# Optimization experiments

Hardware: AMD Instinct MI355X
Metric: run time of the kernel (lower is better)

## Reference

```python
import jax, jax.numpy as jnp
from jax import lax
import numpy as np

B, T, V, H = 64, 256, 4096, 512


def setup_inputs() -> dict:
    key = jax.random.key(0)
    k1, k2, k3, k4 = jax.random.split(key, 4)
    x = jax.random.randint(k1, (B, T), 0, V, dtype=jnp.int32)
    # RNNScratch params (std=0.01 normal init, as in the LM head)
    Wxh = 0.01 * jax.random.normal(k2, (V, H), dtype=jnp.float32)
    Whh = 0.01 * jax.random.normal(k3, (H, H), dtype=jnp.float32)
    bh = jnp.zeros((H,), dtype=jnp.float32)
    Wo = 0.01 * jax.random.normal(k4, (H, V), dtype=jnp.float32)
    Bo = jnp.zeros((V,), dtype=jnp.float32)
    return {"x": x, "Wxh": Wxh, "Whh": Whh, "bh": bh, "Wo": Wo, "Bo": Bo}


def reference(x, Wxh, Whh, bh, Wo, Bo):
    # one_hot(x).float() @ Wxh is exactly a row gather from Wxh
    xs = jnp.take(Wxh, x.T, axis=0)  # [T, B, H]
    h0 = jnp.zeros((x.shape[0], Whh.shape[0]), dtype=Wxh.dtype)

    def step(h, xt):
        h = jnp.tanh(xt + h @ Whh + bh)  # [B, H]
        return h, h

    _, hs = lax.scan(step, h0, xs)  # hs: [T, B, H]
    # per-step output projection, fused into one einsum over time
    out = jnp.einsum("tbh,hv->btv", hs, Wo) + Bo  # [B, T, V]
    return out
```

## Files before the change

kernel.cpp:

```cpp
#include <hip/hip_runtime.h>


typedef __fp16 half2_t __attribute__((ext_vector_type(2)));
typedef __attribute__((ext_vector_type(8))) short short8;
typedef __attribute__((ext_vector_type(4))) float f32x4;

__device__ __forceinline__ unsigned short f32_to_bf16(float f) {
  unsigned int u = __builtin_bit_cast(unsigned int, f);
  u = (u + 0x7FFFu + ((u >> 16) & 1u)) >> 16;
  return (unsigned short)u;
}

__device__ __forceinline__ unsigned int pack_f16x2(float a, float b) {
  half2_t h = __builtin_amdgcn_cvt_pkrtz(a, b);
  return __builtin_bit_cast(unsigned int, h);
}

__device__ __forceinline__ float fdot2_(unsigned int w, unsigned int h, float acc) {
  return __builtin_amdgcn_fdot2(__builtin_bit_cast(half2_t, w),
                                __builtin_bit_cast(half2_t, h), acc, false);
}

__device__ __forceinline__ void glds16(const void* g, void* lds) {
  __builtin_amdgcn_global_load_lds(
      (const __attribute__((address_space(1))) unsigned int*)g,
      (__attribute__((address_space(3))) unsigned int*)lds, 16, 0, 0);
}

__global__ __launch_bounds__(256) void pack_whhB(const float* __restrict__ Whh,
                                                 unsigned int* __restrict__ WhhB,
                                                 unsigned long long* __restrict__ hG64) {
  int idx = blockIdx.x * 256 + threadIdx.x;
  int e = idx & 3;
  int G = idx >> 2;
  int c = G & 127;
  int u = (G >> 7) & 15;
  int q = (G >> 11) & 3;
  int s = G >> 13;
  int p = q * 64 + u * 4 + e;
  int j = s * 128 + c;
  float f0 = Whh[(2 * p) * 512 + j];
  float f1 = Whh[(2 * p + 1) * 512 + j];
  WhhB[idx] = pack_f16x2(f0, f1);
  if (idx < 32768) hG64[idx] = 0ull;
}

__global__ __launch_bounds__(256) void transpose_wo(const float* __restrict__ Wo,
                                                    unsigned short* __restrict__ WoT) {
  __shared__ float tile[64][65];
  const int tv = blockIdx.x;
  const int th = blockIdx.y;
  const int tid = threadIdx.x;
  const int c = tid & 63, r4 = tid >> 6;
#pragma unroll
  for (int p = 0; p < 16; ++p) {
    int hl = p * 4 + r4;
    tile[hl][c] = Wo[(size_t)(th * 64 + hl) * 4096 + tv * 64 + c];
  }
  __syncthreads();
#pragma unroll
  for (int p = 0; p < 16; ++p) {
    int vl = p * 4 + r4;
    WoT[(size_t)(tv * 64 + vl) * 512 + th * 64 + c] = f32_to_bf16(tile[c][vl]);
  }
}

#define DOTK(kc_, A) do { \
  const uint4 w_ = wlds[(kc_) * 128 + c]; \
  const uint4 h_ = hbuf[(kc_)]; \
  A = fdot2_(w_.x, h_.x, A); A = fdot2_(w_.y, h_.y, A); \
  A = fdot2_(w_.z, h_.z, A); A = fdot2_(w_.w, h_.w, A); } while (0)

__global__ __launch_bounds__(512) void rnn_scanD(const int* __restrict__ x,
                                                 const float* __restrict__ Wxh,
                                                 const unsigned int* __restrict__ WhhB,
                                                 const float* __restrict__ bh,
                                                 unsigned short* __restrict__ hs,
                                                 unsigned long long* hG64) {
  __shared__ uint4 wlds[8192];
  __shared__ uint4 hbuf[64];
  __shared__ float pbuf[512];
  __shared__ int toks[256];
  const int bid = blockIdx.x;
  const int s = bid & 3;
  const int b = bid >> 2;
  const int tid = threadIdx.x;
  const int c = tid & 127;
  const int q = tid >> 7;
  const int s16 = s * 16;
  const uint4* W4 = (const uint4*)WhhB;

#pragma unroll
  for (int it = 0; it < 16; ++it) {
    int L = it * 512 + tid;
    wlds[L] = W4[s * 8192 + L];
  }
  if (tid < 64) hbuf[tid] = make_uint4(0u, 0u, 0u, 0u);
  if (tid < 256) toks[tid] = x[b * 256 + tid];
  __syncthreads();

  unsigned int* hb32 = (unsigned int*)hbuf;
  const float bhj = (tid < 128) ? bh[s * 128 + tid] : 0.f;

  for (int t = 0; t < 256; ++t) {
    const int tok = toks[t];
    const float xv = (tid < 128) ? Wxh[(size_t)tok * 512 + s * 128 + tid] : 0.f;

    float a0 = 0.f, a1 = 0.f, a2 = 0.f, a3 = 0.f;
    DOTK(s16 + 0 + q, a0); DOTK(s16 + 4 + q, a1);
    DOTK(s16 + 8 + q, a2); DOTK(s16 + 12 + q, a3);

    if (t > 0 && tid < 192) {
      const int r = (tid < s * 64) ? tid : tid + 64;
      const unsigned long long* src =
          hG64 + (((size_t)(t & 1)) << 14) + b * 256 + r;
      unsigned long long v;
      do {
        v = __hip_atomic_load(src, __ATOMIC_RELAXED, __HIP_MEMORY_SCOPE_AGENT);
      } while ((unsigned)(v >> 32) != (unsigned)t);
      half2_t up = __builtin_bit_cast(half2_t, (unsigned)v);
      hb32[r] = pack_f16x2(tanhf((float)up.x), tanhf((float)up.y));
    }
    __syncthreads();

    {
      int m1 = ((s + 1) & 3) * 16;
      DOTK(m1 + 0 + q, a0); DOTK(m1 + 4 + q, a1);
      DOTK(m1 + 8 + q, a2); DOTK(m1 + 12 + q, a3);
      int m2 = ((s + 2) & 3) * 16;
      DOTK(m2 + 0 + q, a0); DOTK(m2 + 4 + q, a1);
      DOTK(m2 + 8 + q, a2); DOTK(m2 + 12 + q, a3);
      int m3 = ((s + 3) & 3) * 16;
      DOTK(m3 + 0 + q, a0); DOTK(m3 + 4 + q, a1);
      DOTK(m3 + 8 + q, a2); DOTK(m3 + 12 + q, a3);
    }
    pbuf[q * 128 + c] = (a0 + a1) + (a2 + a3);
    __syncthreads();

    if (tid < 128) {
      const float ssum = pbuf[tid] + pbuf[tid + 128] + pbuf[tid + 256] + pbuf[tid + 384];
      const float u1 = xv + ssum + bhj;
      const float u2 = __shfl_down(u1, 1);
      if (!(tid & 1)) {
        const unsigned int up = pack_f16x2(u1, u2);
        __hip_atomic_store(
            hG64 + (((size_t)((t + 1) & 1)) << 14) + b * 256 + 64 * s + (tid >> 1),
            ((unsigned long long)(unsigned)(t + 1) << 32) | up,
            __ATOMIC_RELAXED, __HIP_MEMORY_SCOPE_AGENT);
        half2_t uo = __builtin_bit_cast(half2_t, up);
        const float h1 = tanhf((float)uo.x);
        const float h2 = tanhf((float)uo.y);
        hb32[64 * s + (tid >> 1)] = pack_f16x2(h1, h2);
        ((unsigned int*)hs)[(size_t)(b * 256 + t) * 256 + 64 * s + (tid >> 1)] =
            (unsigned int)f32_to_bf16(h1) | ((unsigned int)f32_to_bf16(h2) << 16);
      }
    }
    __syncthreads();
  }
}

__global__ __launch_bounds__(256) void gemm_out(const unsigned short* __restrict__ A,
                                                const unsigned short* __restrict__ Bt,
                                                const float* __restrict__ Bo,
                                                float* __restrict__ C) {
  __shared__ alignas(16) unsigned short As[128 * 32];
  __shared__ alignas(16) unsigned short Bs[128 * 32];
  const int tid = threadIdx.x;
  const int lane = tid & 63, wid = tid >> 6;
  const int bn = blockIdx.x & 31, bm = blockIdx.x >> 5;
  const int wr = wid >> 1, wc = wid & 1;

  f32x4 acc[4][4] = {};

  const unsigned short* Ag = A + (size_t)(bm * 128 + (tid >> 2)) * 512 + (tid & 3) * 8;
  const unsigned short* Bg = Bt + (size_t)(bn * 128 + (tid >> 2)) * 512 + (tid & 3) * 8;
  char* AsW = (char*)As + wid * 1024;
  char* BsW = (char*)Bs + wid * 1024;

  const int laneRow = lane & 15;
  const int k0 = (lane >> 4) * 8;

  for (int kt = 0; kt < 16; ++kt) {
    __syncthreads();
    const unsigned short* a0 = Ag + kt * 32;
    const unsigned short* b0 = Bg + kt * 32;
    glds16(a0,            AsW);
    glds16(a0 + 64 * 512, AsW + 4096);
    glds16(b0,            BsW);
    glds16(b0 + 64 * 512, BsW + 4096);
    __syncthreads();

    short8 af[4], bf[4];
#pragma unroll
    for (int f = 0; f < 4; ++f)
      af[f] = *(const short8*)&As[(wr * 64 + f * 16 + laneRow) * 32 + k0];
#pragma unroll
    for (int f = 0; f < 4; ++f)
      bf[f] = *(const short8*)&Bs[(wc * 64 + f * 16 + laneRow) * 32 + k0];
#pragma unroll
    for (int fm = 0; fm < 4; ++fm)
#pragma unroll
      for (int fn = 0; fn < 4; ++fn)
        acc[fm][fn] = __builtin_amdgcn_mfma_f32_16x16x32_bf16(af[fm], bf[fn], acc[fm][fn], 0, 0, 0);
  }

  const int mg0 = bm * 128 + wr * 64, ng0 = bn * 128 + wc * 64;
#pragma unroll
  for (int fn = 0; fn < 4; ++fn) {
    const int col = ng0 + fn * 16 + laneRow;
    const float bo = Bo[col];
#pragma unroll
    for (int fm = 0; fm < 4; ++fm) {
      const int row0 = mg0 + fm * 16 + (lane >> 4) * 4;
#pragma unroll
      for (int r = 0; r < 4; ++r)
        C[(size_t)(row0 + r) * 4096 + col] = acc[fm][fn][r] + bo;
    }
  }
}

extern "C" void kernel_launch(void* const* d_in, const int* in_sizes, int n_in,
                              void* d_out, int out_size, void* d_ws, size_t ws_size,
                              hipStream_t stream) {
  (void)in_sizes; (void)n_in; (void)out_size; (void)ws_size;
  const int* x = (const int*)d_in[0];
  const float* Wxh = (const float*)d_in[1];
  const float* Whh = (const float*)d_in[2];
  const float* bh = (const float*)d_in[3];
  const float* Wo = (const float*)d_in[4];
  const float* Bo = (const float*)d_in[5];
  float* out = (float*)d_out;

  unsigned int* WhhB = (unsigned int*)d_ws;
  unsigned short* WoT = (unsigned short*)((char*)d_ws + 524288);
  unsigned short* hs = (unsigned short*)((char*)d_ws + 4718592);
  unsigned long long* hG64 = (unsigned long long*)((char*)d_ws + 21495808);

  hipLaunchKernelGGL(pack_whhB, dim3(512), dim3(256), 0, stream, Whh, WhhB, hG64);
  hipLaunchKernelGGL(transpose_wo, dim3(64, 8), dim3(256), 0, stream, Wo, WoT);
  hipLaunchKernelGGL(rnn_scanD, dim3(256), dim3(512), 0, stream, x, Wxh, WhhB, bh,
                     hs, hG64);
  hipLaunchKernelGGL(gemm_out, dim3(4096), dim3(256), 0, stream, hs, WoT, Bo, out);
}
```

Before: 518.0 us.

## Quantize Whh to fp8 e5m2 and split recurrence across two blocks per batch

Packs Whh as 8-bit e5m2 values, which halves its size, so each block can hold 256 output columns of Whh in LDS. The recurrent scan then uses 2 blocks per batch row instead of 4, and less cross-block handoff is needed each time step. At dot time the fp8 bytes are widened to fp16 by shifting and masking before fdot2. The work is split so one half of the threads computes the local-h contribution while the other half polls the peer block's partial sums. This trades accuracy of Whh, since e5m2 keeps only two mantissa bits, for less inter-block synchronization and fewer launched blocks.

```diff
diff --git a/kernel.cpp b/kernel.cpp
--- a/kernel.cpp
+++ b/kernel.cpp
@@ -27,21 +27,29 @@
       (__attribute__((address_space(3))) unsigned int*)lds, 16, 0, 0);
 }
 
-__global__ __launch_bounds__(256) void pack_whhB(const float* __restrict__ Whh,
-                                                 unsigned int* __restrict__ WhhB,
+__device__ __forceinline__ unsigned int q8_e5m2(float f) {
+  _Float16 hv = (_Float16)f;
+  unsigned short u = __builtin_bit_cast(unsigned short, hv);
+  return (unsigned int)(((unsigned int)u + 0x7Fu + ((u >> 8) & 1u)) >> 8) & 0xFFu;
+}
+
+__global__ __launch_bounds__(256) void pack_whhE(const float* __restrict__ Whh,
+                                                 unsigned int* __restrict__ WhhE,
                                                  unsigned long long* __restrict__ hG64) {
   int idx = blockIdx.x * 256 + threadIdx.x;
-  int e = idx & 3;
+  int d = idx & 3;
   int G = idx >> 2;
-  int c = G & 127;
-  int u = (G >> 7) & 15;
-  int q = (G >> 11) & 3;
+  int c = G & 255;
+  int u = (G >> 8) & 15;
+  int q2 = (G >> 12) & 1;
   int s = G >> 13;
-  int p = q * 64 + u * 4 + e;
-  int j = s * 128 + c;
-  float f0 = Whh[(2 * p) * 512 + j];
-  float f1 = Whh[(2 * p + 1) * 512 + j];
-  WhhB[idx] = pack_f16x2(f0, f1);
+  int m0 = q2 * 128 + u * 8 + 2 * d;
+  int j = s * 256 + c;
+  unsigned int b0 = q8_e5m2(Whh[(2 * m0 + 0) * 512 + j]);
+  unsigned int b2 = q8_e5m2(Whh[(2 * m0 + 1) * 512 + j]);
+  unsigned int b1 = q8_e5m2(Whh[(2 * m0 + 2) * 512 + j]);
+  unsigned int b3 = q8_e5m2(Whh[(2 * m0 + 3) * 512 + j]);
+  WhhE[idx] = b0 | (b1 << 8) | (b2 << 16) | (b3 << 24);
   if (idx < 32768) hG64[idx] = 0ull;
 }
 
@@ -65,53 +73,65 @@
   }
 }
 
-#define DOTK(kc_, A) do { \
-  const uint4 w_ = wlds[(kc_) * 128 + c]; \
-  const uint4 h_ = hbuf[(kc_)]; \
-  A = fdot2_(w_.x, h_.x, A); A = fdot2_(w_.y, h_.y, A); \
-  A = fdot2_(w_.z, h_.z, A); A = fdot2_(w_.w, h_.w, A); } while (0)
-
-__global__ __launch_bounds__(512) void rnn_scanD(const int* __restrict__ x,
+#define DOTCH(u_) do { \
+  const uint4 w_ = wl[(q2 * 16 + (u_)) * 256 + c]; \
+  const uint4 hA = hbuf[q2 * 32 + 2 * (u_)]; \
+  const uint4 hB = hbuf[q2 * 32 + 2 * (u_) + 1]; \
+  unsigned int lo_, hi_; \
+  lo_ = (w_.x << 8) & 0xFF00FF00u; hi_ = w_.x & 0xFF00FF00u; \
+  a0 = fdot2_(lo_, hA.x, a0); a1 = fdot2_(hi_, hA.y, a1); \
+  lo_ = (w_.y << 8) & 0xFF00FF00u; hi_ = w_.y & 0xFF00FF00u; \
+  a2 = fdot2_(lo_, hA.z, a2); a3 = fdot2_(hi_, hA.w, a3); \
+  lo_ = (w_.z << 8) & 0xFF00FF00u; hi_ = w_.z & 0xFF00FF00u; \
+  a0 = fdot2_(lo_, hB.x, a0); a1 = fdot2_(hi_, hB.y, a1); \
+  lo_ = (w_.w << 8) & 0xFF00FF00u; hi_ = w_.w & 0xFF00FF00u; \
+  a2 = fdot2_(lo_, hB.z, a2); a3 = fdot2_(hi_, hB.w, a3); } while (0)
+
+#define DOTALL() do { \
+  DOTCH(0);  DOTCH(1);  DOTCH(2);  DOTCH(3); \
+  DOTCH(4);  DOTCH(5);  DOTCH(6);  DOTCH(7); \
+  DOTCH(8);  DOTCH(9);  DOTCH(10); DOTCH(11); \
+  DOTCH(12); DOTCH(13); DOTCH(14); DOTCH(15); } while (0)
+
+__global__ __launch_bounds__(512) void rnn_scanE(const int* __restrict__ x,
                                                  const float* __restrict__ Wxh,
-                                                 const unsigned int* __restrict__ WhhB,
+                                                 const unsigned int* __restrict__ WhhE,
                                                  const float* __restrict__ bh,
                                                  unsigned short* __restrict__ hs,
                                                  unsigned long long* hG64) {
-  __shared__ uint4 wlds[8192];
+  __shared__ uint4 wl[8192];
   __shared__ uint4 hbuf[64];
   __shared__ float pbuf[512];
   __shared__ int toks[256];
   const int bid = blockIdx.x;
-  const int s = bid & 3;
-  const int b = bid >> 2;
+  const int s = bid & 1;
+  const int b = bid >> 1;
   const int tid = threadIdx.x;
-  const int c = tid & 127;
-  const int q = tid >> 7;
-  const int s16 = s * 16;
-  const uint4* W4 = (const uint4*)WhhB;
+  const int c = tid & 255;
+  const int q2 = tid >> 8;
+  const uint4* W4E = (const uint4*)WhhE;
 
 #pragma unroll
   for (int it = 0; it < 16; ++it) {
     int L = it * 512 + tid;
-    wlds[L] = W4[s * 8192 + L];
+    wl[L] = W4E[s * 8192 + L];
   }
   if (tid < 64) hbuf[tid] = make_uint4(0u, 0u, 0u, 0u);
   if (tid < 256) toks[tid] = x[b * 256 + tid];
   __syncthreads();
 
   unsigned int* hb32 = (unsigned int*)hbuf;
-  const float bhj = (tid < 128) ? bh[s * 128 + tid] : 0.f;
+  const float bhj = (tid < 256) ? bh[s * 256 + tid] : 0.f;
 
   for (int t = 0; t < 256; ++t) {
     const int tok = toks[t];
-    const float xv = (tid < 128) ? Wxh[(size_t)tok * 512 + s * 128 + tid] : 0.f;
+    const float xv = (tid < 256) ? Wxh[(size_t)tok * 512 + s * 256 + tid] : 0.f;
 
     float a0 = 0.f, a1 = 0.f, a2 = 0.f, a3 = 0.f;
-    DOTK(s16 + 0 + q, a0); DOTK(s16 + 4 + q, a1);
-    DOTK(s16 + 8 + q, a2); DOTK(s16 + 12 + q, a3);
-
-    if (t > 0 && tid < 192) {
-      const int r = (tid < s * 64) ? tid : tid + 64;
+    if (q2 == s) {
+      DOTALL();
+    } else if (t > 0 && (tid & 255) < 128) {
+      const int r = 128 * (1 - s) + (tid & 127);
       const unsigned long long* src =
           hG64 + (((size_t)(t & 1)) << 14) + b * 256 + r;
       unsigned long long v;
@@ -123,35 +143,25 @@
     }
     __syncthreads();
 
-    {
-      int m1 = ((s + 1) & 3) * 16;
-      DOTK(m1 + 0 + q, a0); DOTK(m1 + 4 + q, a1);
-      DOTK(m1 + 8 + q, a2); DOTK(m1 + 12 + q, a3);
-      int m2 = ((s + 2) & 3) * 16;
-      DOTK(m2 + 0 + q, a0); DOTK(m2 + 4 + q, a1);
-      DOTK(m2 + 8 + q, a2); DOTK(m2 + 12 + q, a3);
-      int m3 = ((s + 3) & 3) * 16;
-      DOTK(m3 + 0 + q, a0); DOTK(m3 + 4 + q, a1);
-      DOTK(m3 + 8 + q, a2); DOTK(m3 + 12 + q, a3);
-    }
-    pbuf[q * 128 + c] = (a0 + a1) + (a2 + a3);
-    __syncthreads();
-
-    if (tid < 128) {
-      const float ssum = pbuf[tid] + pbuf[tid + 128] + pbuf[tid + 256] + pbuf[tid + 384];
+    if (q2 != s) DOTALL();
+    pbuf[q2 * 256 + c] = (a0 + a1) + (a2 + a3);
+    __syncthreads();
+
+    if (tid < 256) {
+      const float ssum = pbuf[tid] + pbuf[256 + tid];
       const float u1 = xv + ssum + bhj;
       const float u2 = __shfl_down(u1, 1);
       if (!(tid & 1)) {
         const unsigned int up = pack_f16x2(u1, u2);
         __hip_atomic_store(
-            hG64 + (((size_t)((t + 1) & 1)) << 14) + b * 256 + 64 * s + (tid >> 1),
+            hG64 + (((size_t)((t + 1) & 1)) << 14) + b * 256 + 128 * s + (tid >> 1),
             ((unsigned long long)(unsigned)(t + 1) << 32) | up,
             __ATOMIC_RELAXED, __HIP_MEMORY_SCOPE_AGENT);
         half2_t uo = __builtin_bit_cast(half2_t, up);
         const float h1 = tanhf((float)uo.x);
         const float h2 = tanhf((float)uo.y);
-        hb32[64 * s + (tid >> 1)] = pack_f16x2(h1, h2);
-        ((unsigned int*)hs)[(size_t)(b * 256 + t) * 256 + 64 * s + (tid >> 1)] =
+        hb32[128 * s + (tid >> 1)] = pack_f16x2(h1, h2);
+        ((unsigned int*)hs)[(size_t)(b * 256 + t) * 256 + 128 * s + (tid >> 1)] =
             (unsigned int)f32_to_bf16(h1) | ((unsigned int)f32_to_bf16(h2) << 16);
       }
     }
@@ -231,14 +241,14 @@
   const float* Bo = (const float*)d_in[5];
   float* out = (float*)d_out;
 
-  unsigned int* WhhB = (unsigned int*)d_ws;
-  unsigned short* WoT = (unsigned short*)((char*)d_ws + 524288);
-  unsigned short* hs = (unsigned short*)((char*)d_ws + 4718592);
-  unsigned long long* hG64 = (unsigned long long*)((char*)d_ws + 21495808);
-
-  hipLaunchKernelGGL(pack_whhB, dim3(512), dim3(256), 0, stream, Whh, WhhB, hG64);
+  unsigned int* WhhE = (unsigned int*)d_ws;
+  unsigned short* WoT = (unsigned short*)((char*)d_ws + 262144);
+  unsigned short* hs = (unsigned short*)((char*)d_ws + 4456448);
+  unsigned long long* hG64 = (unsigned long long*)((char*)d_ws + 21233664);
+
+  hipLaunchKernelGGL(pack_whhE, dim3(256), dim3(256), 0, stream, Whh, WhhE, hG64);
   hipLaunchKernelGGL(transpose_wo, dim3(64, 8), dim3(256), 0, stream, Wo, WoT);
-  hipLaunchKernelGGL(rnn_scanD, dim3(256), dim3(512), 0, stream, x, Wxh, WhhB, bh,
+  hipLaunchKernelGGL(rnn_scanE, dim3(128), dim3(512), 0, stream, x, Wxh, WhhE, bh,
                      hs, hG64);
   hipLaunchKernelGGL(gemm_out, dim3(4096), dim3(256), 0, stream, hs, WoT, Bo, out);
 }
```

Result: slower. 812.7 us (+56.9%).

## Store recurrent weights as fp8 e5m2 and unpack to fp16 in dot loop

Applied to the files above, without the earlier changes.

Recurrent weight matrix Whh is quantized to 8-bit e5m2 (top byte of fp16) instead of packed fp16. This halves its LDS footprint and the bytes read from LDS per step. Bytes are expanded back to fp16 pairs with shifts and masks before fdot2. This trades extra ALU work and reduced weight precision for lower LDS bandwidth in the latency-bound sequential scan.

```diff
diff --git a/kernel.cpp b/kernel.cpp
--- a/kernel.cpp
+++ b/kernel.cpp
@@ -27,21 +27,28 @@
       (__attribute__((address_space(3))) unsigned int*)lds, 16, 0, 0);
 }
 
-__global__ __launch_bounds__(256) void pack_whhB(const float* __restrict__ Whh,
-                                                 unsigned int* __restrict__ WhhB,
-                                                 unsigned long long* __restrict__ hG64) {
+__device__ __forceinline__ unsigned int q8_e5m2(float f) {
+  _Float16 hv = (_Float16)f;
+  unsigned short u = __builtin_bit_cast(unsigned short, hv);
+  return (unsigned int)(((unsigned int)u + 0x7Fu + ((u >> 8) & 1u)) >> 8) & 0xFFu;
+}
+
+__global__ __launch_bounds__(256) void pack_whhE2(const float* __restrict__ Whh,
+                                                  unsigned int* __restrict__ WhhE2,
+                                                  unsigned long long* __restrict__ hG64) {
   int idx = blockIdx.x * 256 + threadIdx.x;
-  int e = idx & 3;
+  int d = idx & 3;
   int G = idx >> 2;
   int c = G & 127;
-  int u = (G >> 7) & 15;
-  int q = (G >> 11) & 3;
-  int s = G >> 13;
-  int p = q * 64 + u * 4 + e;
+  int kappa = (G >> 7) & 31;
+  int s = G >> 12;
+  int m0 = 8 * kappa + 2 * d;
   int j = s * 128 + c;
-  float f0 = Whh[(2 * p) * 512 + j];
-  float f1 = Whh[(2 * p + 1) * 512 + j];
-  WhhB[idx] = pack_f16x2(f0, f1);
+  unsigned int b0 = q8_e5m2(Whh[(2 * m0 + 0) * 512 + j]);
+  unsigned int b2 = q8_e5m2(Whh[(2 * m0 + 1) * 512 + j]);
+  unsigned int b1 = q8_e5m2(Whh[(2 * m0 + 2) * 512 + j]);
+  unsigned int b3 = q8_e5m2(Whh[(2 * m0 + 3) * 512 + j]);
+  WhhE2[idx] = b0 | (b1 << 8) | (b2 << 16) | (b3 << 24);
   if (idx < 32768) hG64[idx] = 0ull;
 }
 
@@ -65,19 +72,27 @@
   }
 }
 
-#define DOTK(kc_, A) do { \
-  const uint4 w_ = wlds[(kc_) * 128 + c]; \
-  const uint4 h_ = hbuf[(kc_)]; \
-  A = fdot2_(w_.x, h_.x, A); A = fdot2_(w_.y, h_.y, A); \
-  A = fdot2_(w_.z, h_.z, A); A = fdot2_(w_.w, h_.w, A); } while (0)
-
-__global__ __launch_bounds__(512) void rnn_scanD(const int* __restrict__ x,
+#define DOTCH(k_) do { \
+  const uint4 w_ = wl[(k_) * 128 + c]; \
+  const uint4 hA = hbuf[2 * (k_)]; \
+  const uint4 hB = hbuf[2 * (k_) + 1]; \
+  unsigned int lo_, hi_; \
+  lo_ = (w_.x << 8) & 0xFF00FF00u; hi_ = w_.x & 0xFF00FF00u; \
+  a0 = fdot2_(lo_, hA.x, a0); a1 = fdot2_(hi_, hA.y, a1); \
+  lo_ = (w_.y << 8) & 0xFF00FF00u; hi_ = w_.y & 0xFF00FF00u; \
+  a2 = fdot2_(lo_, hA.z, a2); a3 = fdot2_(hi_, hA.w, a3); \
+  lo_ = (w_.z << 8) & 0xFF00FF00u; hi_ = w_.z & 0xFF00FF00u; \
+  a0 = fdot2_(lo_, hB.x, a0); a1 = fdot2_(hi_, hB.y, a1); \
+  lo_ = (w_.w << 8) & 0xFF00FF00u; hi_ = w_.w & 0xFF00FF00u; \
+  a2 = fdot2_(lo_, hB.z, a2); a3 = fdot2_(hi_, hB.w, a3); } while (0)
+
+__global__ __launch_bounds__(512) void rnn_scanF(const int* __restrict__ x,
                                                  const float* __restrict__ Wxh,
-                                                 const unsigned int* __restrict__ WhhB,
+                                                 const unsigned int* __restrict__ WhhE2,
                                                  const float* __restrict__ bh,
                                                  unsigned short* __restrict__ hs,
                                                  unsigned long long* hG64) {
-  __shared__ uint4 wlds[8192];
+  __shared__ uint4 wl[4096];
   __shared__ uint4 hbuf[64];
   __shared__ float pbuf[512];
   __shared__ int toks[256];
@@ -87,13 +102,12 @@
   const int tid = threadIdx.x;
   const int c = tid & 127;
   const int q = tid >> 7;
-  const int s16 = s * 16;
-  const uint4* W4 = (const uint4*)WhhB;
-
-#pragma unroll
-  for (int it = 0; it < 16; ++it) {
+  const uint4* W4E = (const uint4*)WhhE2;
+
+#pragma unroll
+  for (int it = 0; it < 8; ++it) {
     int L = it * 512 + tid;
-    wlds[L] = W4[s * 8192 + L];
+    wl[L] = W4E[s * 4096 + L];
   }
   if (tid < 64) hbuf[tid] = make_uint4(0u, 0u, 0u, 0u);
   if (tid < 256) toks[tid] = x[b * 256 + tid];
@@ -107,8 +121,8 @@
     const float xv = (tid < 128) ? Wxh[(size_t)tok * 512 + s * 128 + tid] : 0.f;
 
     float a0 = 0.f, a1 = 0.f, a2 = 0.f, a3 = 0.f;
-    DOTK(s16 + 0 + q, a0); DOTK(s16 + 4 + q, a1);
-    DOTK(s16 + 8 + q, a2); DOTK(s16 + 12 + q, a3);
+    DOTCH(8 * s + 2 * q);
+    DOTCH(8 * s + 2 * q + 1);
 
     if (t > 0 && tid < 192) {
       const int r = (tid < s * 64) ? tid : tid + 64;
@@ -124,15 +138,12 @@
     __syncthreads();
 
     {
-      int m1 = ((s + 1) & 3) * 16;
-      DOTK(m1 + 0 + q, a0); DOTK(m1 + 4 + q, a1);
-      DOTK(m1 + 8 + q, a2); DOTK(m1 + 12 + q, a3);
-      int m2 = ((s + 2) & 3) * 16;
-      DOTK(m2 + 0 + q, a0); DOTK(m2 + 4 + q, a1);
-      DOTK(m2 + 8 + q, a2); DOTK(m2 + 12 + q, a3);
-      int m3 = ((s + 3) & 3) * 16;
-      DOTK(m3 + 0 + q, a0); DOTK(m3 + 4 + q, a1);
-      DOTK(m3 + 8 + q, a2); DOTK(m3 + 12 + q, a3);
+      const int m1 = ((s + 1) & 3) * 8 + 2 * q;
+      DOTCH(m1); DOTCH(m1 + 1);
+      const int m2 = ((s + 2) & 3) * 8 + 2 * q;
+      DOTCH(m2); DOTCH(m2 + 1);
+      const int m3 = ((s + 3) & 3) * 8 + 2 * q;
+      DOTCH(m3); DOTCH(m3 + 1);
     }
     pbuf[q * 128 + c] = (a0 + a1) + (a2 + a3);
     __syncthreads();
@@ -231,14 +242,14 @@
   const float* Bo = (const float*)d_in[5];
   float* out = (float*)d_out;
 
-  unsigned int* WhhB = (unsigned int*)d_ws;
-  unsigned short* WoT = (unsigned short*)((char*)d_ws + 524288);
-  unsigned short* hs = (unsigned short*)((char*)d_ws + 4718592);
-  unsigned long long* hG64 = (unsigned long long*)((char*)d_ws + 21495808);
-
-  hipLaunchKernelGGL(pack_whhB, dim3(512), dim3(256), 0, stream, Whh, WhhB, hG64);
+  unsigned int* WhhE2 = (unsigned int*)d_ws;
+  unsigned short* WoT = (unsigned short*)((char*)d_ws + 262144);
+  unsigned short* hs = (unsigned short*)((char*)d_ws + 4456448);
+  unsigned long long* hG64 = (unsigned long long*)((char*)d_ws + 21233664);
+
+  hipLaunchKernelGGL(pack_whhE2, dim3(256), dim3(256), 0, stream, Whh, WhhE2, hG64);
   hipLaunchKernelGGL(transpose_wo, dim3(64, 8), dim3(256), 0, stream, Wo, WoT);
-  hipLaunchKernelGGL(rnn_scanD, dim3(256), dim3(512), 0, stream, x, Wxh, WhhB, bh,
+  hipLaunchKernelGGL(rnn_scanF, dim3(256), dim3(512), 0, stream, x, Wxh, WhhE2, bh,
                      hs, hG64);
   hipLaunchKernelGGL(gemm_out, dim3(4096), dim3(256), 0, stream, hs, WoT, Bo, out);
 }
```

New measurement: 582.1 us. 12.4% more time.

## Interleave four batch rows per scan block to hide cross-block hidden-state latency

Applied to the files above, without the earlier changes.

The recurrent scan kernel now has each block handle four batch rows in round-robin instead of one, so the grid shrinks from 256 to 64 blocks. While one row waits for its peer blocks' hidden-state slices, the block computes the other rows, and the next row's slot is prefetched with an atomic load. The aim is to hide the inter-block spin-wait latency behind useful work. In exchange, per-row work is serialized within fewer blocks, and the early split of the local-K dot product that previously overlapped the wait is dropped.

```diff
diff --git a/kernel.cpp b/kernel.cpp
--- a/kernel.cpp
+++ b/kernel.cpp
@@ -65,29 +65,29 @@
   }
 }
 
-#define DOTK(kc_, A) do { \
+#define DOTK(hb_, kc_, A) do { \
   const uint4 w_ = wlds[(kc_) * 128 + c]; \
-  const uint4 h_ = hbuf[(kc_)]; \
+  const uint4 h_ = hb_[(kc_)]; \
   A = fdot2_(w_.x, h_.x, A); A = fdot2_(w_.y, h_.y, A); \
   A = fdot2_(w_.z, h_.z, A); A = fdot2_(w_.w, h_.w, A); } while (0)
 
-__global__ __launch_bounds__(512) void rnn_scanD(const int* __restrict__ x,
+__global__ __launch_bounds__(512) void rnn_scanG(const int* __restrict__ x,
                                                  const float* __restrict__ Wxh,
                                                  const unsigned int* __restrict__ WhhB,
                                                  const float* __restrict__ bh,
                                                  unsigned short* __restrict__ hs,
                                                  unsigned long long* hG64) {
   __shared__ uint4 wlds[8192];
-  __shared__ uint4 hbuf[64];
-  __shared__ float pbuf[512];
-  __shared__ int toks[256];
+  __shared__ uint4 hbuf4[4][64];
+  __shared__ float pbuf[4][512];
+  __shared__ int toks[1024];
   const int bid = blockIdx.x;
   const int s = bid & 3;
-  const int b = bid >> 2;
+  const int grp = bid >> 2;
+  const int b0 = grp * 4;
   const int tid = threadIdx.x;
   const int c = tid & 127;
   const int q = tid >> 7;
-  const int s16 = s * 16;
   const uint4* W4 = (const uint4*)WhhB;
 
 #pragma unroll
@@ -95,67 +95,76 @@
     int L = it * 512 + tid;
     wlds[L] = W4[s * 8192 + L];
   }
-  if (tid < 64) hbuf[tid] = make_uint4(0u, 0u, 0u, 0u);
-  if (tid < 256) toks[tid] = x[b * 256 + tid];
+  if (tid < 256) {
+    ((uint4*)hbuf4)[tid] = make_uint4(0u, 0u, 0u, 0u);
+  }
+  for (int i = tid; i < 1024; i += 512) toks[i] = x[b0 * 256 + i];
   __syncthreads();
 
-  unsigned int* hb32 = (unsigned int*)hbuf;
   const float bhj = (tid < 128) ? bh[s * 128 + tid] : 0.f;
+  const int rslot = (tid < s * 64) ? tid : tid + 64;
+
+  unsigned long long vpre = 0ull;
 
   for (int t = 0; t < 256; ++t) {
-    const int tok = toks[t];
-    const float xv = (tid < 128) ? Wxh[(size_t)tok * 512 + s * 128 + tid] : 0.f;
-
-    float a0 = 0.f, a1 = 0.f, a2 = 0.f, a3 = 0.f;
-    DOTK(s16 + 0 + q, a0); DOTK(s16 + 4 + q, a1);
-    DOTK(s16 + 8 + q, a2); DOTK(s16 + 12 + q, a3);
-
-    if (t > 0 && tid < 192) {
-      const int r = (tid < s * 64) ? tid : tid + 64;
-      const unsigned long long* src =
-          hG64 + (((size_t)(t & 1)) << 14) + b * 256 + r;
-      unsigned long long v;
-      do {
-        v = __hip_atomic_load(src, __ATOMIC_RELAXED, __HIP_MEMORY_SCOPE_AGENT);
-      } while ((unsigned)(v >> 32) != (unsigned)t);
-      half2_t up = __builtin_bit_cast(half2_t, (unsigned)v);
-      hb32[r] = pack_f16x2(tanhf((float)up.x), tanhf((float)up.y));
+#pragma unroll
+    for (int n = 0; n < 4; ++n) {
+      const int b = b0 + n;
+      unsigned int* hb32 = (unsigned int*)hbuf4[n];
+      const uint4* hb = hbuf4[n];
+
+      const int tok = toks[n * 256 + t];
+      const float xv = (tid < 128) ? Wxh[(size_t)tok * 512 + s * 128 + tid] : 0.f;
+
+      if (t > 0 && tid < 192) {
+        const unsigned long long* src =
+            hG64 + (((size_t)(t & 1)) << 14) + b * 256 + rslot;
+        unsigned long long v = vpre;
+        while ((unsigned)(v >> 32) != (unsigned)t)
+          v = __hip_atomic_load(src, __ATOMIC_RELAXED, __HIP_MEMORY_SCOPE_AGENT);
+        half2_t up = __builtin_bit_cast(half2_t, (unsigned)v);
+        hb32[rslot] = pack_f16x2(tanhf((float)up.x), tanhf((float)up.y));
+      }
+      if (tid < 192) {
+        const int nn = (n + 1) & 3;
+        const int tt = (n == 3) ? (t + 1) : t;
+        const unsigned long long* psrc =
+            hG64 + (((size_t)(tt & 1)) << 14) + (b0 + nn) * 256 + rslot;
+        vpre = __hip_atomic_load(psrc, __ATOMIC_RELAXED, __HIP_MEMORY_SCOPE_AGENT);
+      }
+      __syncthreads();
+
+      float a0 = 0.f, a1 = 0.f, a2 = 0.f, a3 = 0.f;
+#pragma unroll
+      for (int i = 0; i < 4; ++i) {
+        DOTK(hb, 16 * i + 0 * 4 + q, a0);
+        DOTK(hb, 16 * i + 1 * 4 + q, a1);
+        DOTK(hb, 16 * i + 2 * 4 + q, a2);
+        DOTK(hb, 16 * i + 3 * 4 + q, a3);
+      }
+      pbuf[n][q * 128 + c] = (a0 + a1) + (a2 + a3);
+      __syncthreads();
+
+      if (tid < 128) {
+        const float ssum = pbuf[n][tid] + pbuf[n][tid + 128] +
+                           pbuf[n][tid + 256] + pbuf[n][tid + 384];
+        const float u1 = xv + ssum + bhj;
+        const float u2 = __shfl_down(u1, 1);
+        if (!(tid & 1)) {
+          const unsigned int up = pack_f16x2(u1, u2);
+          __hip_atomic_store(
+              hG64 + (((size_t)((t + 1) & 1)) << 14) + b * 256 + 64 * s + (tid >> 1),
+              ((unsigned long long)(unsigned)(t + 1) << 32) | up,
+              __ATOMIC_RELAXED, __HIP_MEMORY_SCOPE_AGENT);
+          half2_t uo = __builtin_bit_cast(half2_t, up);
+          const float h1 = tanhf((float)uo.x);
+          const float h2 = tanhf((float)uo.y);
+          hb32[64 * s + (tid >> 1)] = pack_f16x2(h1, h2);
+          ((unsigned int*)hs)[(size_t)(b * 256 + t) * 256 + 64 * s + (tid >> 1)] =
+              (unsigned int)f32_to_bf16(h1) | ((unsigned int)f32_to_bf16(h2) << 16);
+        }
+      }
     }
-    __syncthreads();
-
-    {
-      int m1 = ((s + 1) & 3) * 16;
-      DOTK(m1 + 0 + q, a0); DOTK(m1 + 4 + q, a1);
-      DOTK(m1 + 8 + q, a2); DOTK(m1 + 12 + q, a3);
-      int m2 = ((s + 2) & 3) * 16;
-      DOTK(m2 + 0 + q, a0); DOTK(m2 + 4 + q, a1);
-      DOTK(m2 + 8 + q, a2); DOTK(m2 + 12 + q, a3);
-      int m3 = ((s + 3) & 3) * 16;
-      DOTK(m3 + 0 + q, a0); DOTK(m3 + 4 + q, a1);
-      DOTK(m3 + 8 + q, a2); DOTK(m3 + 12 + q, a3);
-    }
-    pbuf[q * 128 + c] = (a0 + a1) + (a2 + a3);
-    __syncthreads();
-
-    if (tid < 128) {
-      const float ssum = pbuf[tid] + pbuf[tid + 128] + pbuf[tid + 256] + pbuf[tid + 384];
-      const float u1 = xv + ssum + bhj;
-      const float u2 = __shfl_down(u1, 1);
-      if (!(tid & 1)) {
-        const unsigned int up = pack_f16x2(u1, u2);
-        __hip_atomic_store(
-            hG64 + (((size_t)((t + 1) & 1)) << 14) + b * 256 + 64 * s + (tid >> 1),
-            ((unsigned long long)(unsigned)(t + 1) << 32) | up,
-            __ATOMIC_RELAXED, __HIP_MEMORY_SCOPE_AGENT);
-        half2_t uo = __builtin_bit_cast(half2_t, up);
-        const float h1 = tanhf((float)uo.x);
-        const float h2 = tanhf((float)uo.y);
-        hb32[64 * s + (tid >> 1)] = pack_f16x2(h1, h2);
-        ((unsigned int*)hs)[(size_t)(b * 256 + t) * 256 + 64 * s + (tid >> 1)] =
-            (unsigned int)f32_to_bf16(h1) | ((unsigned int)f32_to_bf16(h2) << 16);
-      }
-    }
-    __syncthreads();
   }
 }
 
@@ -238,7 +247,7 @@
 
   hipLaunchKernelGGL(pack_whhB, dim3(512), dim3(256), 0, stream, Whh, WhhB, hG64);
   hipLaunchKernelGGL(transpose_wo, dim3(64, 8), dim3(256), 0, stream, Wo, WoT);
-  hipLaunchKernelGGL(rnn_scanD, dim3(256), dim3(512), 0, stream, x, Wxh, WhhB, bh,
+  hipLaunchKernelGGL(rnn_scanG, dim3(64), dim3(512), 0, stream, x, Wxh, WhhB, bh,
                      hs, hG64);
   hipLaunchKernelGGL(gemm_out, dim3(4096), dim3(256), 0, stream, hs, WoT, Bo, out);
 }
```

New measurement: 1.258 ms. 2.43x slower.
